# Optimization experiments

Hardware: AMD Instinct MI355X
Metric: run time of the kernel (lower is better)

The kernel has to match this reference:

```python
import jax, jax.numpy as jnp
import numpy as np

E = 3_200_000  # edges
N = 100_000    # atoms
B = 64         # graphs


def setup_inputs() -> dict:
    key = jax.random.key(0)
    k1, k2, k3, k4 = jax.random.split(key, 4)
    disp = jax.random.normal(k1, (E, 3), dtype=jnp.float32)
    edge_w = jax.random.uniform(k2, (E,), dtype=jnp.float32)
    edge_index = jax.random.randint(k3, (2, E), 0, N)
    batch = jnp.sort(jax.random.randint(k4, (N,), 0, B))
    return {"disp": disp, "edge_w": edge_w, "edge_index": edge_index,
            "batch": batch, "num_graphs": B}


def reference(disp, edge_w, edge_index, batch, num_graphs):
    n_atoms = batch.shape[0]

    # Surrogate differentiable energy of disp (stands in for the upstream model):
    # E = sum_e w_e * ||disp_e||^2. pairwise_force = -dE/ddisp via autodiff,
    # matching torch.autograd.grad(energy, disp).
    def energy_fn(d):
        return jnp.sum(edge_w * jnp.sum(d * d, axis=-1))

    pairwise_force = -jax.grad(energy_fn)(disp)  # (E, 3)

    # Per-edge virial outer product: (E, 3, 3)
    virial_e = disp[:, :, None] * pairwise_force[:, None, :]

    # Double scatter-add to atoms (both endpoints), then scatter to graphs.
    v_atom = (jax.ops.segment_sum(virial_e, edge_index[0], num_segments=n_atoms)
              + jax.ops.segment_sum(virial_e, edge_index[1], num_segments=n_atoms))  # (N,3,3)
    v_graph = jax.ops.segment_sum(v_atom, batch, num_segments=num_graphs)  # (B,3,3)
    return v_graph
```

## Files before the change

kernel.cpp:

```cpp
#include <hip/hip_runtime.h>


#define NG 64
#define NCOMP 6
#define NPART (NG * NCOMP)
#define RED1_BLOCKS 64
#define MFMA_BLOCKS 768
#define WPB 4
#define MROW 72
#define DROW 72

typedef unsigned short u16_t;
typedef unsigned int   u32_t;
typedef __attribute__((ext_vector_type(8))) short short8;
typedef __attribute__((ext_vector_type(4))) float f32x4;

__device__ __forceinline__ u16_t f2bf(float f) {
    union { float f; u32_t u; } v; v.f = f;
    u32_t r = v.u + 0x7FFFu + ((v.u >> 16) & 1u);
    return (u16_t)(r >> 16);
}

__device__ __forceinline__ void lds_add(float* p, float v) {
    __hip_atomic_fetch_add(p, v, __ATOMIC_RELAXED, __HIP_MEMORY_SCOPE_WORKGROUP);
}

__global__ __launch_bounds__(256) void virial_mfma(
    const float* __restrict__ disp, const float* __restrict__ edge_w,
    const int* __restrict__ edge_index, const int* __restrict__ batch,
    float* __restrict__ partials, int E)
{
    __shared__ u16_t Msh[WPB][NG * MROW];
    __shared__ u16_t Dsh[WPB][16 * DROW];

    const int lane = threadIdx.x & 63;
    const int wave = threadIdx.x >> 6;
    u16_t* Mw = Msh[wave];
    u16_t* Dw = Dsh[wave];

    {
        u32_t* p = (u32_t*)Mw;
        for (int i = lane; i < NG * MROW / 2; i += 64) p[i] = 0u;
        u32_t* q = (u32_t*)Dw;
        for (int i = lane; i < 16 * DROW / 2; i += 64) q[i] = 0u;
    }

    f32x4 acc0 = {0,0,0,0}, acc1 = {0,0,0,0}, acc2 = {0,0,0,0}, acc3 = {0,0,0,0};
    const int ngroups = (E + 63) >> 6;
    const int gstride = (int)gridDim.x * WPB;
    const int c_l = lane & 15;
    const int k4  = lane >> 4;
    int pg0 = 0, pg1 = 0;

    int grp = (int)blockIdx.x * WPB + wave;

    int   p_g0 = 0, p_g1 = 0;
    float p_w = 0.f, p_d0 = 0.f, p_d1 = 0.f, p_d2 = 0.f;
    if (grp < ngroups) {
        int e  = grp * 64 + lane;
        int ec = e < E ? e : E - 1;
        p_w  = (e < E) ? edge_w[ec] : 0.f;
        p_d0 = disp[ec * 3 + 0];
        p_d1 = disp[ec * 3 + 1];
        p_d2 = disp[ec * 3 + 2];
        p_g0 = batch[edge_index[ec]];
        p_g1 = batch[edge_index[E + ec]];
    }

    while (grp < ngroups) {
        const int   g0 = p_g0, g1 = p_g1;
        const float w = p_w, d0 = p_d0, d1 = p_d1, d2 = p_d2;

        const int nxt = grp + gstride;
        if (nxt < ngroups) {
            int e  = nxt * 64 + lane;
            int ec = e < E ? e : E - 1;
            p_w  = (e < E) ? edge_w[ec] : 0.f;
            p_d0 = disp[ec * 3 + 0];
            p_d1 = disp[ec * 3 + 1];
            p_d2 = disp[ec * 3 + 2];
            p_g0 = batch[edge_index[ec]];
            p_g1 = batch[edge_index[E + ec]];
        }

        Mw[pg0 * MROW + lane] = 0;
        Mw[pg1 * MROW + lane] = 0;
        Mw[g0 * MROW + lane] = 0x3F80u;
        Mw[g1 * MROW + lane] = (g1 == g0) ? 0x4000u : 0x3F80u;
        pg0 = g0; pg1 = g1;

        float cw = -2.f * w;
        Dw[0 * DROW + lane] = f2bf(cw * d0 * d0);
        Dw[1 * DROW + lane] = f2bf(cw * d0 * d1);
        Dw[2 * DROW + lane] = f2bf(cw * d0 * d2);
        Dw[3 * DROW + lane] = f2bf(cw * d1 * d1);
        Dw[4 * DROW + lane] = f2bf(cw * d1 * d2);
        Dw[5 * DROW + lane] = f2bf(cw * d2 * d2);

#pragma unroll
        for (int half = 0; half < 2; ++half) {
            const int kb = half * 32 + k4 * 8;
            short8 bf = *(const short8*)&Dw[c_l * DROW + kb];
            short8 a0 = *(const short8*)&Mw[( 0 + c_l) * MROW + kb];
            short8 a1 = *(const short8*)&Mw[(16 + c_l) * MROW + kb];
            short8 a2 = *(const short8*)&Mw[(32 + c_l) * MROW + kb];
            short8 a3 = *(const short8*)&Mw[(48 + c_l) * MROW + kb];
            acc0 = __builtin_amdgcn_mfma_f32_16x16x32_bf16(a0, bf, acc0, 0, 0, 0);
            acc1 = __builtin_amdgcn_mfma_f32_16x16x32_bf16(a1, bf, acc1, 0, 0, 0);
            acc2 = __builtin_amdgcn_mfma_f32_16x16x32_bf16(a2, bf, acc2, 0, 0, 0);
            acc3 = __builtin_amdgcn_mfma_f32_16x16x32_bf16(a3, bf, acc3, 0, 0, 0);
        }

        grp = nxt;
    }

    float* Ow = (float*)Dw;
    if (c_l < NCOMP) {
#pragma unroll
        for (int r = 0; r < 4; ++r) {
            Ow[( 0 + k4 * 4 + r) * NCOMP + c_l] = acc0[r];
            Ow[(16 + k4 * 4 + r) * NCOMP + c_l] = acc1[r];
            Ow[(32 + k4 * 4 + r) * NCOMP + c_l] = acc2[r];
            Ow[(48 + k4 * 4 + r) * NCOMP + c_l] = acc3[r];
        }
    }
    __syncthreads();
    for (int i = threadIdx.x; i < NPART; i += blockDim.x) {
        float s = ((const float*)Dsh[0])[i] + ((const float*)Dsh[1])[i]
                + ((const float*)Dsh[2])[i] + ((const float*)Dsh[3])[i];
        partials[(size_t)blockIdx.x * NPART + i] = s;
    }
}

__global__ __launch_bounds__(NPART) void reduce1_kernel(
    const float* __restrict__ partials, float* __restrict__ partials2, int nblk)
{
    int i = threadIdx.x, j = blockIdx.x;
    float s = 0.f;
    for (int b = j; b < nblk; b += RED1_BLOCKS)
        s += partials[(size_t)b * NPART + i];
    partials2[(size_t)j * NPART + i] = s;
}

__global__ __launch_bounds__(NPART) void reduce2_kernel(
    const float* __restrict__ partials2, float* __restrict__ dst)
{
    int i = threadIdx.x;
    float s = 0.f;
#pragma unroll
    for (int j = 0; j < RED1_BLOCKS; ++j)
        s += partials2[(size_t)j * NPART + i];
    int g = i / NCOMP, c = i % NCOMP;
    int r   = (c < 3) ? 0 : ((c < 5) ? 1 : 2);
    int col = (c < 3) ? c : ((c < 5) ? c - 2 : 2);
    dst[g * 9 + r * 3 + col] = s;
    if (r != col) dst[g * 9 + col * 3 + r] = s;
}

__global__ void zero_out_kernel(float* __restrict__ out, int n) {
    int i = blockIdx.x * blockDim.x + threadIdx.x;
    if (i < n) out[i] = 0.f;
}

__global__ __launch_bounds__(256) void virial_atomic(
    const float* __restrict__ disp, const float* __restrict__ edge_w,
    const int* __restrict__ edge_index, const int* __restrict__ batch,
    float* __restrict__ out, int E)
{
    __shared__ float acc[NG * 7];
    for (int i = threadIdx.x; i < NG * 7; i += blockDim.x) acc[i] = 0.f;
    __syncthreads();
    int tid = blockIdx.x * blockDim.x + threadIdx.x;
    int stride = gridDim.x * blockDim.x;
    for (int e = tid; e < E; e += stride) {
        float d0 = disp[e*3], d1 = disp[e*3+1], d2 = disp[e*3+2];
        float c = -2.f * edge_w[e];
        int g0 = batch[edge_index[e]], g1 = batch[edge_index[E + e]];
        float v[6] = {c*d0*d0, c*d0*d1, c*d0*d2, c*d1*d1, c*d1*d2, c*d2*d2};
#pragma unroll
        for (int k = 0; k < 6; ++k) {
            lds_add(&acc[g0*7+k], v[k]);
            lds_add(&acc[g1*7+k], v[k]);
        }
    }
    __syncthreads();
    for (int i = threadIdx.x; i < NG * 9; i += blockDim.x) {
        int g = i / 9, ij = i % 9, r = ij / 3, cc = ij % 3;
        int lo = r < cc ? r : cc, hi = r < cc ? cc : r;
        int comp = (lo == 0) ? hi : ((lo == 1) ? 2 + hi : 5);
        __hip_atomic_fetch_add(&out[i], acc[g*7+comp], __ATOMIC_RELAXED, __HIP_MEMORY_SCOPE_AGENT);
    }
}

extern "C" void kernel_launch(void* const* d_in, const int* in_sizes, int n_in,
                              void* d_out, int out_size, void* d_ws, size_t ws_size,
                              hipStream_t stream) {
    const float* disp       = (const float*)d_in[0];
    const float* edge_w     = (const float*)d_in[1];
    const int*   edge_index = (const int*)d_in[2];
    const int*   batch      = (const int*)d_in[3];
    float*       out        = (float*)d_out;
    const int E = in_sizes[1];

    const size_t need = (size_t)(MFMA_BLOCKS + RED1_BLOCKS) * NPART * sizeof(float);

    if (ws_size >= need) {
        float* pm  = (float*)d_ws;
        float* p2  = pm + (size_t)MFMA_BLOCKS * NPART;

        virial_mfma<<<MFMA_BLOCKS, 256, 0, stream>>>(disp, edge_w, edge_index, batch, pm, E);
        reduce1_kernel<<<RED1_BLOCKS, NPART, 0, stream>>>(pm, p2, MFMA_BLOCKS);
        reduce2_kernel<<<1, NPART, 0, stream>>>(p2, out);
    } else {
        zero_out_kernel<<<1, 256, 0, stream>>>(out, NG * 9);
        virial_atomic<<<2048, 256, 0, stream>>>(disp, edge_w, edge_index, batch, out, E);
    }
}
```

Measured before the change: 44.23 us.

## Share one 128-edge one-hot tile per block across four waves

Each block now loads a 128-edge group with half its threads and writes one shared one-hot matrix and one displacement-product tile. The four waves then each compute a 16-graph slice of the 64 graphs with four MFMAs over K=128. Before, every wave built its own 64-edge tile and ran all four row tiles. This removes the per-block cross-wave sum, cuts LDS footprint per block, and raises the grid to 1792 blocks. In exchange it adds two block-wide barriers per iteration and leaves half the threads idle during loads.

```diff
diff --git a/kernel.cpp b/kernel.cpp
--- a/kernel.cpp
+++ b/kernel.cpp
@@ -5,10 +5,10 @@
 #define NCOMP 6
 #define NPART (NG * NCOMP)
 #define RED1_BLOCKS 64
-#define MFMA_BLOCKS 768
-#define WPB 4
-#define MROW 72
-#define DROW 72
+#define MFMA_BLOCKS 1792
+#define GE 128
+#define MROW 136
+#define DROW 136
 
 typedef unsigned short u16_t;
 typedef unsigned int   u32_t;
@@ -30,34 +30,35 @@
     const int* __restrict__ edge_index, const int* __restrict__ batch,
     float* __restrict__ partials, int E)
 {
-    __shared__ u16_t Msh[WPB][NG * MROW];
-    __shared__ u16_t Dsh[WPB][16 * DROW];
-
-    const int lane = threadIdx.x & 63;
-    const int wave = threadIdx.x >> 6;
-    u16_t* Mw = Msh[wave];
-    u16_t* Dw = Dsh[wave];
+    __shared__ u16_t M [NG * MROW];
+    __shared__ u16_t Dt[16 * DROW];
+
+    const int t    = threadIdx.x;
+    const int lane = t & 63;
+    const int wave = t >> 6;
+    const int c_l  = lane & 15;
+    const int k4   = lane >> 4;
 
     {
-        u32_t* p = (u32_t*)Mw;
-        for (int i = lane; i < NG * MROW / 2; i += 64) p[i] = 0u;
-        u32_t* q = (u32_t*)Dw;
-        for (int i = lane; i < 16 * DROW / 2; i += 64) q[i] = 0u;
-    }
-
-    f32x4 acc0 = {0,0,0,0}, acc1 = {0,0,0,0}, acc2 = {0,0,0,0}, acc3 = {0,0,0,0};
-    const int ngroups = (E + 63) >> 6;
-    const int gstride = (int)gridDim.x * WPB;
-    const int c_l = lane & 15;
-    const int k4  = lane >> 4;
+        u32_t* p = (u32_t*)M;
+        for (int i = t; i < NG * MROW / 2; i += 256) p[i] = 0u;
+        u32_t* q = (u32_t*)Dt;
+        for (int i = t; i < 16 * DROW / 2; i += 256) q[i] = 0u;
+    }
+    __syncthreads();
+
+    f32x4 acc = {0.f, 0.f, 0.f, 0.f};
+    const int  ngroups = (E + GE - 1) / GE;
+    const int  gstride = (int)gridDim.x;
+    const bool loader  = (t < GE);
+
+    int grp = (int)blockIdx.x;
     int pg0 = 0, pg1 = 0;
-
-    int grp = (int)blockIdx.x * WPB + wave;
 
     int   p_g0 = 0, p_g1 = 0;
     float p_w = 0.f, p_d0 = 0.f, p_d1 = 0.f, p_d2 = 0.f;
-    if (grp < ngroups) {
-        int e  = grp * 64 + lane;
+    if (loader && grp < ngroups) {
+        int e  = grp * GE + t;
         int ec = e < E ? e : E - 1;
         p_w  = (e < E) ? edge_w[ec] : 0.f;
         p_d0 = disp[ec * 3 + 0];
@@ -70,10 +71,28 @@
     while (grp < ngroups) {
         const int   g0 = p_g0, g1 = p_g1;
         const float w = p_w, d0 = p_d0, d1 = p_d1, d2 = p_d2;
-
-        const int nxt = grp + gstride;
-        if (nxt < ngroups) {
-            int e  = nxt * 64 + lane;
+        const int   nxt = grp + gstride;
+
+        __syncthreads();
+        if (loader) {
+            M[pg0 * MROW + t] = 0;
+            M[pg1 * MROW + t] = 0;
+            M[g0 * MROW + t] = 0x3F80u;
+            M[g1 * MROW + t] = (g1 == g0) ? 0x4000u : 0x3F80u;
+            pg0 = g0; pg1 = g1;
+
+            float cw = -2.f * w;
+            Dt[0 * DROW + t] = f2bf(cw * d0 * d0);
+            Dt[1 * DROW + t] = f2bf(cw * d0 * d1);
+            Dt[2 * DROW + t] = f2bf(cw * d0 * d2);
+            Dt[3 * DROW + t] = f2bf(cw * d1 * d1);
+            Dt[4 * DROW + t] = f2bf(cw * d1 * d2);
+            Dt[5 * DROW + t] = f2bf(cw * d2 * d2);
+        }
+        __syncthreads();
+
+        if (loader && nxt < ngroups) {
+            int e  = nxt * GE + t;
             int ec = e < E ? e : E - 1;
             p_w  = (e < E) ? edge_w[ec] : 0.f;
             p_d0 = disp[ec * 3 + 0];
@@ -83,53 +102,27 @@
             p_g1 = batch[edge_index[E + ec]];
         }
 
-        Mw[pg0 * MROW + lane] = 0;
-        Mw[pg1 * MROW + lane] = 0;
-        Mw[g0 * MROW + lane] = 0x3F80u;
-        Mw[g1 * MROW + lane] = (g1 == g0) ? 0x4000u : 0x3F80u;
-        pg0 = g0; pg1 = g1;
-
-        float cw = -2.f * w;
-        Dw[0 * DROW + lane] = f2bf(cw * d0 * d0);
-        Dw[1 * DROW + lane] = f2bf(cw * d0 * d1);
-        Dw[2 * DROW + lane] = f2bf(cw * d0 * d2);
-        Dw[3 * DROW + lane] = f2bf(cw * d1 * d1);
-        Dw[4 * DROW + lane] = f2bf(cw * d1 * d2);
-        Dw[5 * DROW + lane] = f2bf(cw * d2 * d2);
-
-#pragma unroll
-        for (int half = 0; half < 2; ++half) {
-            const int kb = half * 32 + k4 * 8;
-            short8 bf = *(const short8*)&Dw[c_l * DROW + kb];
-            short8 a0 = *(const short8*)&Mw[( 0 + c_l) * MROW + kb];
-            short8 a1 = *(const short8*)&Mw[(16 + c_l) * MROW + kb];
-            short8 a2 = *(const short8*)&Mw[(32 + c_l) * MROW + kb];
-            short8 a3 = *(const short8*)&Mw[(48 + c_l) * MROW + kb];
-            acc0 = __builtin_amdgcn_mfma_f32_16x16x32_bf16(a0, bf, acc0, 0, 0, 0);
-            acc1 = __builtin_amdgcn_mfma_f32_16x16x32_bf16(a1, bf, acc1, 0, 0, 0);
-            acc2 = __builtin_amdgcn_mfma_f32_16x16x32_bf16(a2, bf, acc2, 0, 0, 0);
-            acc3 = __builtin_amdgcn_mfma_f32_16x16x32_bf16(a3, bf, acc3, 0, 0, 0);
+#pragma unroll
+        for (int q = 0; q < 4; ++q) {
+            const int kb = q * 32 + k4 * 8;
+            short8 bf = *(const short8*)&Dt[c_l * DROW + kb];
+            short8 af = *(const short8*)&M[(16 * wave + c_l) * MROW + kb];
+            acc = __builtin_amdgcn_mfma_f32_16x16x32_bf16(af, bf, acc, 0, 0, 0);
         }
 
         grp = nxt;
     }
 
-    float* Ow = (float*)Dw;
+    __syncthreads();
+    float* Osh = (float*)Dt;
     if (c_l < NCOMP) {
 #pragma unroll
-        for (int r = 0; r < 4; ++r) {
-            Ow[( 0 + k4 * 4 + r) * NCOMP + c_l] = acc0[r];
-            Ow[(16 + k4 * 4 + r) * NCOMP + c_l] = acc1[r];
-            Ow[(32 + k4 * 4 + r) * NCOMP + c_l] = acc2[r];
-            Ow[(48 + k4 * 4 + r) * NCOMP + c_l] = acc3[r];
-        }
-    }
-    __syncthreads();
-    for (int i = threadIdx.x; i < NPART; i += blockDim.x) {
-        float s = ((const float*)Dsh[0])[i] + ((const float*)Dsh[1])[i]
-                + ((const float*)Dsh[2])[i] + ((const float*)Dsh[3])[i];
-        partials[(size_t)blockIdx.x * NPART + i] = s;
-    }
+        for (int r = 0; r < 4; ++r)
+            Osh[(16 * wave + k4 * 4 + r) * NCOMP + c_l] = acc[r];
+    }
+    __syncthreads();
+    for (int i = t; i < NPART; i += 256)
+        partials[(size_t)blockIdx.x * NPART + i] = Osh[i];
 }
 
 __global__ __launch_bounds__(NPART) void reduce1_kernel(
@@ -202,14 +195,17 @@
     float*       out        = (float*)d_out;
     const int E = in_sizes[1];
 
-    const size_t need = (size_t)(MFMA_BLOCKS + RED1_BLOCKS) * NPART * sizeof(float);
+    int ngroups = (E + GE - 1) / GE;
+    int nblk = MFMA_BLOCKS < ngroups ? MFMA_BLOCKS : ngroups;
+
+    const size_t need = (size_t)(nblk + RED1_BLOCKS) * NPART * sizeof(float);
 
     if (ws_size >= need) {
-        float* pm  = (float*)d_ws;
-        float* p2  = pm + (size_t)MFMA_BLOCKS * NPART;
-
-        virial_mfma<<<MFMA_BLOCKS, 256, 0, stream>>>(disp, edge_w, edge_index, batch, pm, E);
-        reduce1_kernel<<<RED1_BLOCKS, NPART, 0, stream>>>(pm, p2, MFMA_BLOCKS);
+        float* pm = (float*)d_ws;
+        float* p2 = pm + (size_t)nblk * NPART;
+
+        virial_mfma<<<nblk, 256, 0, stream>>>(disp, edge_w, edge_index, batch, pm, E);
+        reduce1_kernel<<<RED1_BLOCKS, NPART, 0, stream>>>(pm, p2, nblk);
         reduce2_kernel<<<1, NPART, 0, stream>>>(p2, out);
     } else {
         zero_out_kernel<<<1, 256, 0, stream>>>(out, NG * 9);
```

Measured after the change: 48.37 us. 9.4% more time.

## Vectorize edge loads into 256-edge macro-groups with shuffle redistribution

Applied to the files above, without the earlier changes.

Each wave now processes 256 contiguous edges per iteration. Every lane loads 4 consecutive edges with float4/int4 vector loads, and the gathered graph ids are packed into one int. Wave shuffles and selects then hand the data back to the original 64-edge-per-step MFMA layout. The aim is fewer, wider global load instructions and more memory traffic in flight per prefetch. The cost is many extra shuffle instructions and higher register pressure, and the packing assumes graph ids fit in 8 bits.

```diff
diff --git a/kernel.cpp b/kernel.cpp
--- a/kernel.cpp
+++ b/kernel.cpp
@@ -21,9 +21,52 @@
     return (u16_t)(r >> 16);
 }
 
+__device__ __forceinline__ float sel4f(float a, float b, float c, float d, int k) {
+    float ab = (k & 1) ? b : a;
+    float cd = (k & 1) ? d : c;
+    return (k & 2) ? cd : ab;
+}
+__device__ __forceinline__ int sel4i(int a, int b, int c, int d, int k) {
+    int ab = (k & 1) ? b : a;
+    int cd = (k & 1) ? d : c;
+    return (k & 2) ? cd : ab;
+}
+
 __device__ __forceinline__ void lds_add(float* p, float v) {
     __hip_atomic_fetch_add(p, v, __ATOMIC_RELAXED, __HIP_MEMORY_SCOPE_WORKGROUP);
 }
+
+#define LOADQ(MAC, W, X, Y, Z, GP) do {                                        \
+    int eb_ = (MAC) * 256 + 4 * lane;                                          \
+    if (((MAC) + 1) * 256 <= E) {                                              \
+        float4 w4_ = *(const float4*)&edge_w[eb_];                             \
+        float4 dA_ = *(const float4*)&disp[eb_ * 3 + 0];                       \
+        float4 dB_ = *(const float4*)&disp[eb_ * 3 + 4];                       \
+        float4 dC_ = *(const float4*)&disp[eb_ * 3 + 8];                       \
+        int4   s4_ = *(const int4*)&edge_index[eb_];                           \
+        int4   t4_ = *(const int4*)&edge_index[E + eb_];                       \
+        W[0] = w4_.x; W[1] = w4_.y; W[2] = w4_.z; W[3] = w4_.w;                \
+        X[0] = dA_.x; Y[0] = dA_.y; Z[0] = dA_.z;                              \
+        X[1] = dA_.w; Y[1] = dB_.x; Z[1] = dB_.y;                              \
+        X[2] = dB_.z; Y[2] = dB_.w; Z[2] = dC_.x;                              \
+        X[3] = dC_.y; Y[3] = dC_.z; Z[3] = dC_.w;                              \
+        GP[0] = batch[s4_.x] | (batch[t4_.x] << 8);                            \
+        GP[1] = batch[s4_.y] | (batch[t4_.y] << 8);                            \
+        GP[2] = batch[s4_.z] | (batch[t4_.z] << 8);                            \
+        GP[3] = batch[s4_.w] | (batch[t4_.w] << 8);                            \
+    } else {                                                                   \
+        _Pragma("unroll")                                                      \
+        for (int k_ = 0; k_ < 4; ++k_) {                                       \
+            int e_  = eb_ + k_;                                                \
+            int ec_ = e_ < E ? e_ : E - 1;                                     \
+            W[k_] = (e_ < E) ? edge_w[ec_] : 0.f;                              \
+            X[k_] = disp[ec_ * 3 + 0];                                         \
+            Y[k_] = disp[ec_ * 3 + 1];                                         \
+            Z[k_] = disp[ec_ * 3 + 2];                                         \
+            GP[k_] = batch[edge_index[ec_]] | (batch[edge_index[E + ec_]] << 8);\
+        }                                                                      \
+    }                                                                          \
+} while (0)
 
 __global__ __launch_bounds__(256) void virial_mfma(
     const float* __restrict__ disp, const float* __restrict__ edge_w,
@@ -32,7 +75,6 @@
 {
     __shared__ u16_t Msh[WPB][NG * MROW];
     __shared__ u16_t Dsh[WPB][16 * DROW];
-
     const int lane = threadIdx.x & 63;
     const int wave = threadIdx.x >> 6;
     u16_t* Mw = Msh[wave];
@@ -46,72 +88,76 @@
     }
 
     f32x4 acc0 = {0,0,0,0}, acc1 = {0,0,0,0}, acc2 = {0,0,0,0}, acc3 = {0,0,0,0};
-    const int ngroups = (E + 63) >> 6;
-    const int gstride = (int)gridDim.x * WPB;
+    const int nmacros = (E + 255) >> 8;
+    const int mstride = (int)gridDim.x * WPB;
     const int c_l = lane & 15;
     const int k4  = lane >> 4;
+    const int ksel = lane & 3;
     int pg0 = 0, pg1 = 0;
 
-    int grp = (int)blockIdx.x * WPB + wave;
-
-    int   p_g0 = 0, p_g1 = 0;
-    float p_w = 0.f, p_d0 = 0.f, p_d1 = 0.f, p_d2 = 0.f;
-    if (grp < ngroups) {
-        int e  = grp * 64 + lane;
-        int ec = e < E ? e : E - 1;
-        p_w  = (e < E) ? edge_w[ec] : 0.f;
-        p_d0 = disp[ec * 3 + 0];
-        p_d1 = disp[ec * 3 + 1];
-        p_d2 = disp[ec * 3 + 2];
-        p_g0 = batch[edge_index[ec]];
-        p_g1 = batch[edge_index[E + ec]];
-    }
-
-    while (grp < ngroups) {
-        const int   g0 = p_g0, g1 = p_g1;
-        const float w = p_w, d0 = p_d0, d1 = p_d1, d2 = p_d2;
-
-        const int nxt = grp + gstride;
-        if (nxt < ngroups) {
-            int e  = nxt * 64 + lane;
-            int ec = e < E ? e : E - 1;
-            p_w  = (e < E) ? edge_w[ec] : 0.f;
-            p_d0 = disp[ec * 3 + 0];
-            p_d1 = disp[ec * 3 + 1];
-            p_d2 = disp[ec * 3 + 2];
-            p_g0 = batch[edge_index[ec]];
-            p_g1 = batch[edge_index[E + ec]];
-        }
-
-        Mw[pg0 * MROW + lane] = 0;
-        Mw[pg1 * MROW + lane] = 0;
-        Mw[g0 * MROW + lane] = 0x3F80u;
-        Mw[g1 * MROW + lane] = (g1 == g0) ? 0x4000u : 0x3F80u;
-        pg0 = g0; pg1 = g1;
-
-        float cw = -2.f * w;
-        Dw[0 * DROW + lane] = f2bf(cw * d0 * d0);
-        Dw[1 * DROW + lane] = f2bf(cw * d0 * d1);
-        Dw[2 * DROW + lane] = f2bf(cw * d0 * d2);
-        Dw[3 * DROW + lane] = f2bf(cw * d1 * d1);
-        Dw[4 * DROW + lane] = f2bf(cw * d1 * d2);
-        Dw[5 * DROW + lane] = f2bf(cw * d2 * d2);
-
-#pragma unroll
-        for (int half = 0; half < 2; ++half) {
-            const int kb = half * 32 + k4 * 8;
-            short8 bf = *(const short8*)&Dw[c_l * DROW + kb];
-            short8 a0 = *(const short8*)&Mw[( 0 + c_l) * MROW + kb];
-            short8 a1 = *(const short8*)&Mw[(16 + c_l) * MROW + kb];
-            short8 a2 = *(const short8*)&Mw[(32 + c_l) * MROW + kb];
-            short8 a3 = *(const short8*)&Mw[(48 + c_l) * MROW + kb];
-            acc0 = __builtin_amdgcn_mfma_f32_16x16x32_bf16(a0, bf, acc0, 0, 0, 0);
-            acc1 = __builtin_amdgcn_mfma_f32_16x16x32_bf16(a1, bf, acc1, 0, 0, 0);
-            acc2 = __builtin_amdgcn_mfma_f32_16x16x32_bf16(a2, bf, acc2, 0, 0, 0);
-            acc3 = __builtin_amdgcn_mfma_f32_16x16x32_bf16(a3, bf, acc3, 0, 0, 0);
-        }
-
-        grp = nxt;
+    int mac = (int)blockIdx.x * WPB + wave;
+
+    float nw[4] = {0,0,0,0}, nx[4] = {0,0,0,0}, ny[4] = {0,0,0,0}, nz[4] = {0,0,0,0};
+    int   ngp[4] = {0,0,0,0};
+    if (mac < nmacros) LOADQ(mac, nw, nx, ny, nz, ngp);
+
+    while (mac < nmacros) {
+        float aw[4], ax[4], ay[4], az[4];
+        int   agp[4];
+#pragma unroll
+        for (int k = 0; k < 4; ++k) {
+            aw[k] = nw[k]; ax[k] = nx[k]; ay[k] = ny[k]; az[k] = nz[k];
+            agp[k] = ngp[k];
+        }
+        const int nxt = mac + mstride;
+        if (nxt < nmacros) LOADQ(nxt, nw, nx, ny, nz, ngp);
+
+#pragma unroll
+        for (int j = 0; j < 4; ++j) {
+            const int src = 16 * j + (lane >> 2);
+            float wv = sel4f(__shfl(aw[0], src), __shfl(aw[1], src),
+                             __shfl(aw[2], src), __shfl(aw[3], src), ksel);
+            float xv = sel4f(__shfl(ax[0], src), __shfl(ax[1], src),
+                             __shfl(ax[2], src), __shfl(ax[3], src), ksel);
+            float yv = sel4f(__shfl(ay[0], src), __shfl(ay[1], src),
+                             __shfl(ay[2], src), __shfl(ay[3], src), ksel);
+            float zv = sel4f(__shfl(az[0], src), __shfl(az[1], src),
+                             __shfl(az[2], src), __shfl(az[3], src), ksel);
+            int  gpv = sel4i(__shfl(agp[0], src), __shfl(agp[1], src),
+                             __shfl(agp[2], src), __shfl(agp[3], src), ksel);
+            const int g0 = gpv & 0xFF;
+            const int g1 = (gpv >> 8) & 0xFF;
+
+            Mw[pg0 * MROW + lane] = 0;
+            Mw[pg1 * MROW + lane] = 0;
+            Mw[g0 * MROW + lane] = 0x3F80u;
+            Mw[g1 * MROW + lane] = (g1 == g0) ? 0x4000u : 0x3F80u;
+            pg0 = g0; pg1 = g1;
+
+            float cwv = -2.f * wv;
+            Dw[0 * DROW + lane] = f2bf(cwv * xv * xv);
+            Dw[1 * DROW + lane] = f2bf(cwv * xv * yv);
+            Dw[2 * DROW + lane] = f2bf(cwv * xv * zv);
+            Dw[3 * DROW + lane] = f2bf(cwv * yv * yv);
+            Dw[4 * DROW + lane] = f2bf(cwv * yv * zv);
+            Dw[5 * DROW + lane] = f2bf(cwv * zv * zv);
+
+#pragma unroll
+            for (int half = 0; half < 2; ++half) {
+                const int kb = half * 32 + k4 * 8;
+                short8 bf = *(const short8*)&Dw[c_l * DROW + kb];
+                short8 a0 = *(const short8*)&Mw[( 0 + c_l) * MROW + kb];
+                short8 a1 = *(const short8*)&Mw[(16 + c_l) * MROW + kb];
+                short8 a2 = *(const short8*)&Mw[(32 + c_l) * MROW + kb];
+                short8 a3 = *(const short8*)&Mw[(48 + c_l) * MROW + kb];
+                acc0 = __builtin_amdgcn_mfma_f32_16x16x32_bf16(a0, bf, acc0, 0, 0, 0);
+                acc1 = __builtin_amdgcn_mfma_f32_16x16x32_bf16(a1, bf, acc1, 0, 0, 0);
+                acc2 = __builtin_amdgcn_mfma_f32_16x16x32_bf16(a2, bf, acc2, 0, 0, 0);
+                acc3 = __builtin_amdgcn_mfma_f32_16x16x32_bf16(a3, bf, acc3, 0, 0, 0);
+            }
+        }
+
+        mac = nxt;
     }
 
     float* Ow = (float*)Dw;
@@ -205,8 +251,8 @@
     const size_t need = (size_t)(MFMA_BLOCKS + RED1_BLOCKS) * NPART * sizeof(float);
 
     if (ws_size >= need) {
-        float* pm  = (float*)d_ws;
-        float* p2  = pm + (size_t)MFMA_BLOCKS * NPART;
+        float* pm = (float*)d_ws;
+        float* p2 = pm + (size_t)MFMA_BLOCKS * NPART;
 
         virial_mfma<<<MFMA_BLOCKS, 256, 0, stream>>>(disp, edge_w, edge_index, batch, pm, E);
         reduce1_kernel<<<RED1_BLOCKS, NPART, 0, stream>>>(pm, p2, MFMA_BLOCKS);
```

After: 53.67 us. 21.3% more time.

## Replace per-edge batch gather with binary search over sorted graph boundaries

Applied to the files above, without the earlier changes.

Three small kernels compute the starting atom index of each graph from the sorted batch array. The main kernel keeps these 65 boundaries in LDS and finds each endpoint's graph with a 6-step binary search, replacing the dependent gather through batch. This removes a random global load per endpoint at the cost of extra ALU/LDS work and three extra kernel launches. It relies on batch being sorted, which the reference input guarantees.

```diff
diff --git a/kernel.cpp b/kernel.cpp
--- a/kernel.cpp
+++ b/kernel.cpp
@@ -25,25 +25,61 @@
     __hip_atomic_fetch_add(p, v, __ATOMIC_RELAXED, __HIP_MEMORY_SCOPE_WORKGROUP);
 }
 
+__device__ __forceinline__ int gsearch(const int* Bs, int a) {
+    int lo = 0;
+#pragma unroll
+    for (int st = 32; st >= 1; st >>= 1)
+        lo += (Bs[lo + st] <= a) ? st : 0;
+    return lo;
+}
+
+__global__ void bounds_init(int* __restrict__ B, int N) {
+    int i = threadIdx.x;
+    if (i < 65) B[i] = N;
+}
+
+__global__ __launch_bounds__(256) void bounds_min(
+    const int* __restrict__ batch, int* __restrict__ B, int N)
+{
+    __shared__ int lb[64];
+    int t = threadIdx.x;
+    if (t < 64) lb[t] = N;
+    __syncthreads();
+    for (int i = blockIdx.x * blockDim.x + t; i < N; i += gridDim.x * blockDim.x)
+        atomicMin(&lb[batch[i]], i);
+    __syncthreads();
+    if (t < 64 && lb[t] < N) atomicMin(&B[t], lb[t]);
+}
+
+__global__ void bounds_fix(int* __restrict__ B) {
+    if (threadIdx.x == 0) {
+        for (int g = 63; g >= 0; --g)
+            if (B[g] > B[g + 1]) B[g] = B[g + 1];
+    }
+}
+
 __global__ __launch_bounds__(256) void virial_mfma(
     const float* __restrict__ disp, const float* __restrict__ edge_w,
-    const int* __restrict__ edge_index, const int* __restrict__ batch,
+    const int* __restrict__ edge_index, const int* __restrict__ Bg,
     float* __restrict__ partials, int E)
 {
     __shared__ u16_t Msh[WPB][NG * MROW];
     __shared__ u16_t Dsh[WPB][16 * DROW];
+    __shared__ int   Bs[65];
 
     const int lane = threadIdx.x & 63;
     const int wave = threadIdx.x >> 6;
     u16_t* Mw = Msh[wave];
     u16_t* Dw = Dsh[wave];
 
+    if (threadIdx.x < 65) Bs[threadIdx.x] = Bg[threadIdx.x];
     {
         u32_t* p = (u32_t*)Mw;
         for (int i = lane; i < NG * MROW / 2; i += 64) p[i] = 0u;
         u32_t* q = (u32_t*)Dw;
         for (int i = lane; i < 16 * DROW / 2; i += 64) q[i] = 0u;
     }
+    __syncthreads();
 
     f32x4 acc0 = {0,0,0,0}, acc1 = {0,0,0,0}, acc2 = {0,0,0,0}, acc3 = {0,0,0,0};
     const int ngroups = (E + 63) >> 6;
@@ -54,34 +90,37 @@
 
     int grp = (int)blockIdx.x * WPB + wave;
 
-    int   p_g0 = 0, p_g1 = 0;
-    float p_w = 0.f, p_d0 = 0.f, p_d1 = 0.f, p_d2 = 0.f;
+    float pw = 0.f, px = 0.f, py = 0.f, pz = 0.f;
+    int   ps = 0, pt = 0;
     if (grp < ngroups) {
         int e  = grp * 64 + lane;
         int ec = e < E ? e : E - 1;
-        p_w  = (e < E) ? edge_w[ec] : 0.f;
-        p_d0 = disp[ec * 3 + 0];
-        p_d1 = disp[ec * 3 + 1];
-        p_d2 = disp[ec * 3 + 2];
-        p_g0 = batch[edge_index[ec]];
-        p_g1 = batch[edge_index[E + ec]];
+        pw = (e < E) ? edge_w[ec] : 0.f;
+        px = disp[ec * 3 + 0];
+        py = disp[ec * 3 + 1];
+        pz = disp[ec * 3 + 2];
+        ps = edge_index[ec];
+        pt = edge_index[E + ec];
     }
 
     while (grp < ngroups) {
-        const int   g0 = p_g0, g1 = p_g1;
-        const float w = p_w, d0 = p_d0, d1 = p_d1, d2 = p_d2;
+        const float w = pw, d0 = px, d1 = py, d2 = pz;
+        const int   sC = ps, tC = pt;
 
         const int nxt = grp + gstride;
         if (nxt < ngroups) {
             int e  = nxt * 64 + lane;
             int ec = e < E ? e : E - 1;
-            p_w  = (e < E) ? edge_w[ec] : 0.f;
-            p_d0 = disp[ec * 3 + 0];
-            p_d1 = disp[ec * 3 + 1];
-            p_d2 = disp[ec * 3 + 2];
-            p_g0 = batch[edge_index[ec]];
-            p_g1 = batch[edge_index[E + ec]];
-        }
+            pw = (e < E) ? edge_w[ec] : 0.f;
+            px = disp[ec * 3 + 0];
+            py = disp[ec * 3 + 1];
+            pz = disp[ec * 3 + 2];
+            ps = edge_index[ec];
+            pt = edge_index[E + ec];
+        }
+
+        const int g0 = gsearch(Bs, sC);
+        const int g1 = gsearch(Bs, tC);
 
         Mw[pg0 * MROW + lane] = 0;
         Mw[pg1 * MROW + lane] = 0;
@@ -201,14 +240,20 @@
     const int*   batch      = (const int*)d_in[3];
     float*       out        = (float*)d_out;
     const int E = in_sizes[1];
-
-    const size_t need = (size_t)(MFMA_BLOCKS + RED1_BLOCKS) * NPART * sizeof(float);
+    const int N = in_sizes[3];
+
+    const size_t need = (size_t)(MFMA_BLOCKS + RED1_BLOCKS) * NPART * sizeof(float)
+                        + 128 * sizeof(int);
 
     if (ws_size >= need) {
-        float* pm  = (float*)d_ws;
-        float* p2  = pm + (size_t)MFMA_BLOCKS * NPART;
-
-        virial_mfma<<<MFMA_BLOCKS, 256, 0, stream>>>(disp, edge_w, edge_index, batch, pm, E);
+        float* pm = (float*)d_ws;
+        float* p2 = pm + (size_t)MFMA_BLOCKS * NPART;
+        int*   B  = (int*)(p2 + (size_t)RED1_BLOCKS * NPART);
+
+        bounds_init<<<1, 128, 0, stream>>>(B, N);
+        bounds_min<<<256, 256, 0, stream>>>(batch, B, N);
+        bounds_fix<<<1, 64, 0, stream>>>(B);
+        virial_mfma<<<MFMA_BLOCKS, 256, 0, stream>>>(disp, edge_w, edge_index, B, pm, E);
         reduce1_kernel<<<RED1_BLOCKS, NPART, 0, stream>>>(pm, p2, MFMA_BLOCKS);
         reduce2_kernel<<<1, NPART, 0, stream>>>(p2, out);
     } else {
```

After: 47.53 us. +7.5%, slower.
